# Kernel tuning notes

Hardware: AMD Instinct MI355X
Metric: run time of the kernel (lower is better)

The kernel has to match this reference:

```python
import jax, jax.numpy as jnp
import numpy as np

DECAY = 0.99
EPS = 1e-5  # Laplace smoothing eps in cluster-size balancing


def _quantize(z_flat, embedding, cluster_size, emb_avg, n_codes):
    # z_flat: [N, D]; embedding: [K, D]
    d = (jnp.sum(z_flat * z_flat, axis=1, keepdims=True)
         + jnp.sum(embedding * embedding, axis=1)
         - 2.0 * (z_flat @ embedding.T))                      # [N, K]
    idx = jnp.argmin(d, axis=1)                               # [N]
    # EMA update (training path). segment_sum == one-hot matmul scatter-add.
    counts = jax.ops.segment_sum(jnp.ones(z_flat.shape[0], z_flat.dtype), idx,
                                 num_segments=n_codes)        # [K]
    new_cs = cluster_size * DECAY + (1.0 - DECAY) * counts
    dw = jax.ops.segment_sum(z_flat, idx, num_segments=n_codes)  # [K, D]
    new_avg = emb_avg * DECAY + (1.0 - DECAY) * dw
    n = new_cs.sum()
    bal = (new_cs + EPS) / (n + n_codes * EPS) * n
    # torch assigns via .data (no autograd) -> stop_gradient for faithfulness
    new_emb = jax.lax.stop_gradient(new_avg / bal[:, None])
    z_q = jnp.take(new_emb, idx, axis=0)  # == one_hot(idx) @ new_emb
    return idx, z_q


def _l2norm(x):
    # F.normalize(x, dim=-1) with eps=1e-12
    return x / jnp.maximum(jnp.linalg.norm(x, axis=-1, keepdims=True), 1e-12)


def reference(z, structure_embedding, style_embedding,
              structure_cluster_size, style_cluster_size,
              structure_embedding_avg, style_embedding_avg):
    b, c, h, w, d = z.shape
    zp = jnp.transpose(z, (0, 2, 3, 4, 1))      # b h w d c
    z_flat = zp.reshape(-1, c)                  # [N, D]
    s_idx, s_q = _quantize(z_flat, structure_embedding, structure_cluster_size,
                           structure_embedding_avg, structure_embedding.shape[0])
    y_idx, y_q = _quantize(z_flat, style_embedding, style_cluster_size,
                           style_embedding_avg, style_embedding.shape[0])

    def back(q):  # [N, C] -> b c h w d
        return jnp.transpose(q.reshape(b, h, w, d, c), (0, 4, 1, 2, 3))

    s_enc = back(s_q)
    y_enc = back(y_q)
    # NOTE: faithful to source — normalize over LAST axis of (b,c,h,w,d),
    # i.e. the spatial depth axis, exactly as F.normalize(dim=-1) does there.
    dis = jnp.mean(jnp.sum(_l2norm(s_enc) * _l2norm(y_enc), axis=-1) ** 2)
    z_q = (s_enc + y_enc) * 0.5
    return z_q, dis, s_idx, y_idx


def setup_inputs() -> dict:
    key = jax.random.key(0)
    k1, k2, k3 = jax.random.split(key, 3)
    B, C, H, W, D = 16, 256, 16, 16, 16
    Ks, Ky = 1024, 512
    return {
        "z": jax.random.normal(k1, (B, C, H, W, D), dtype=jnp.float32),
        "structure_embedding": jax.random.normal(k2, (Ks, C), dtype=jnp.float32),
        "style_embedding": jax.random.normal(k3, (Ky, C), dtype=jnp.float32),
        "structure_cluster_size": jnp.zeros((Ks,), jnp.float32),
        "style_cluster_size": jnp.zeros((Ky,), jnp.float32),
        "structure_embedding_avg": jnp.zeros((Ks, C), jnp.float32),
        "style_embedding_avg": jnp.zeros((Ky, C), jnp.float32),
    }
```

## Files before the change

kernel.cpp:

```cpp
#include <hip/hip_runtime.h>
#include <float.h>

#define NROWS 65536
#define CDIM  256
#define KS    1024
#define KY    512
#define KTOT  1536
#define SPB   4096

#define WB_CNT_S       0
#define WB_CNT_Y       4096
#define WB_RESCUE_CNT  6144
#define WB_DISACC      6152
#define WB_DW_S        6400
#define WB_DW_Y        1054976
#define WB_ZERO_BYTES  1579264
#define WB_EIMG        1579264
#define WB_EN2         2365696
#define WB_IDXS_I      2371840
#define WB_IDXY_I      2633984
#define WB_RLIST_S     2896128
#define WB_RLIST_Y     3158272
#define WB_BASE_S      3420416
#define WB_BASE_Y      3424512
#define WB_CUR_S       3426560
#define WB_CUR_Y       3430656
#define WB_SCALE_S     3432704
#define WB_SCALE_Y     3436800
#define WB_PERM_S      3438848
#define WB_PERM_Y      3700992
#define WB_KSORT_S     3963136
#define WB_KSORT_Y     4225280
#define WB_EMB_S       4487424
#define WB_EMB_Y       5536000

#define OFF_OUT_ZQ   0
#define OFF_OUT_DIS  16777216
#define OFF_OUT_SIDX 16777217
#define OFF_OUT_YIDX 16842753

typedef __attribute__((ext_vector_type(8)))  _Float16 f16x8;
typedef __attribute__((ext_vector_type(4)))  float    f32x4;

__device__ __forceinline__ unsigned int umn(unsigned int a, unsigned int b) { return a < b ? a : b; }
__device__ __forceinline__ unsigned int umx(unsigned int a, unsigned int b) { return a > b ? a : b; }

__global__ void prep_e(const float* __restrict__ Es, const float* __restrict__ Ey,
                       unsigned short* __restrict__ eimg, float* __restrict__ en2) {
    int k = blockIdx.x;
    int lane = threadIdx.x;
    const float* E = (k < KS) ? (Es + (size_t)k * CDIM) : (Ey + (size_t)(k - KS) * CDIM);
    float4 v = *(const float4*)(E + lane * 4);
    float nrm = v.x * v.x + v.y * v.y + v.z * v.z + v.w * v.w;
#pragma unroll
    for (int off = 32; off > 0; off >>= 1) nrm += __shfl_down(nrm, off);
    if (lane == 0) en2[k] = nrm;

    unsigned short q0 = __builtin_bit_cast(unsigned short, (_Float16)v.x);
    unsigned short q1 = __builtin_bit_cast(unsigned short, (_Float16)v.y);
    unsigned short q2 = __builtin_bit_cast(unsigned short, (_Float16)v.z);
    unsigned short q3 = __builtin_bit_cast(unsigned short, (_Float16)v.w);
    uint2 hp = make_uint2((unsigned)q0 | ((unsigned)q1 << 16),
                          (unsigned)q2 | ((unsigned)q3 << 16));

    int c0 = lane * 4;
    int kc = c0 >> 5, g = (c0 >> 3) & 3, j0 = c0 & 7;
    size_t byteoff = (size_t)(k >> 4) * 8192 + (size_t)kc * 1024
                   + (size_t)(g * 16 + (k & 15)) * 16 + (size_t)j0 * 2;
    *(uint2*)((char*)eimg + byteoff) = hp;
}

__global__ void prep_z(const float* __restrict__ z, float* __restrict__ zf) {
    __shared__ float Zs[32][257];
    int blk = blockIdx.x;
    int n0 = blk * 32, b = n0 >> 12, s0 = n0 & 4095;
    int t = threadIdx.x;
    const float* zb = z + (size_t)b * CDIM * SPB + s0;
#pragma unroll
    for (int i = 0; i < 32; ++i) {
        int l = i * 256 + t;
        int c = l >> 5, s = l & 31;
        Zs[s][c] = zb[(size_t)c * SPB + s];
    }
    __syncthreads();
#pragma unroll
    for (int j = 0; j < 8; ++j) {
        int gid = j * 256 + t;
        int nl = gid >> 6, fg = gid & 63;
        float4 v = *(const float4*)(&Zs[nl][fg * 4]);
        *(float4*)(&zf[(size_t)(n0 + nl) * 256 + fg * 4]) = v;
    }
}

__device__ __forceinline__ void stage_phase(const unsigned short* __restrict__ eimg,
                                            int phase, char* lsbase, int wave, int lane) {
    const char* gs = (const char*)eimg + (size_t)phase * 16384 + (size_t)(wave * 2) * 1024 + lane * 16;
    char* ls = lsbase + wave * 2 * 1024;
#pragma unroll
    for (int i = 0; i < 2; ++i)
        __builtin_amdgcn_global_load_lds(
            (const __attribute__((address_space(1))) void*)(gs + i * 1024),
            (__attribute__((address_space(3))) void*)(ls + i * 1024), 16, 0, 0);
}

__launch_bounds__(512, 2)
__global__ void assign_kernel(const float* __restrict__ zf, const unsigned short* __restrict__ eimg,
                              const float* __restrict__ en2,
                              float* __restrict__ sidx_f, float* __restrict__ yidx_f,
                              int* __restrict__ sidx_i, int* __restrict__ yidx_i,
                              int* __restrict__ cnt_s, int* __restrict__ cnt_y,
                              int* __restrict__ rescue_cnt,
                              int* __restrict__ rlist_s, int* __restrict__ rlist_y) {
    __shared__ char sh[4][16384];
    const int tid = threadIdx.x, wave = tid >> 6, lane = tid & 63;
    const int n0 = blockIdx.x * 256;

    f16x8 A[2][8];
#pragma unroll
    for (int rg = 0; rg < 2; ++rg) {
        const float* zr = zf + (size_t)(n0 + wave * 32 + rg * 16 + (lane & 15)) * 256
                        + (lane >> 4) * 8;
#pragma unroll
        for (int kc = 0; kc < 8; ++kc) {
            float4 f0 = *(const float4*)(zr + kc * 32);
            float4 f1 = *(const float4*)(zr + kc * 32 + 4);
            f16x8 a;
            a[0] = (_Float16)f0.x; a[1] = (_Float16)f0.y;
            a[2] = (_Float16)f0.z; a[3] = (_Float16)f0.w;
            a[4] = (_Float16)f1.x; a[5] = (_Float16)f1.y;
            a[6] = (_Float16)f1.z; a[7] = (_Float16)f1.w;
            A[rg][kc] = a;
        }
    }

    stage_phase(eimg, 0, &sh[0][0], wave, lane);
    stage_phase(eimg, 1, &sh[1][0], wave, lane);

    unsigned int m1a[2][4], m2a[2][4];
#pragma unroll
    for (int rg = 0; rg < 2; ++rg)
#pragma unroll
        for (int q = 0; q < 4; ++q) { m1a[rg][q] = 0xFFFFFFFFu; m2a[rg][q] = 0xFFFFFFFFu; }

    for (int p = 0; p < 48; ++p) {
        if (p + 2 < 48) stage_phase(eimg, p + 2, &sh[(p + 2) & 3][0], wave, lane);
        if (p < 46)       asm volatile("s_waitcnt vmcnt(4)" ::: "memory");
        else if (p == 46) asm volatile("s_waitcnt vmcnt(2)" ::: "memory");
        else              asm volatile("s_waitcnt vmcnt(0)" ::: "memory");
        __builtin_amdgcn_s_barrier();
        asm volatile("" ::: "memory");

#pragma unroll
        for (int c = 0; c < 2; ++c) {
            const char* cb = &sh[p & 3][c * 8192] + lane * 16;
            f32x4 acc0 = {}, acc1 = {};
#pragma unroll
            for (int kc = 0; kc < 8; ++kc) {
                f16x8 B = *(const f16x8*)(cb + kc * 1024);
                acc0 = __builtin_amdgcn_mfma_f32_16x16x32_f16(A[0][kc], B, acc0, 0, 0, 0);
                acc1 = __builtin_amdgcn_mfma_f32_16x16x32_f16(A[1][kc], B, acc1, 0, 0, 0);
            }
            const int kcode = p * 32 + c * 16 + (lane & 15);
            const float en0 = en2[kcode] + 512.0f;
            const unsigned int tag = (unsigned int)kcode;
#pragma unroll
            for (int q = 0; q < 4; ++q) {
                float d0 = fmaf(-2.f, acc0[q], en0);
                unsigned int du0 = (__float_as_uint(d0) & 0xFFFFF800u) | tag;
                m2a[0][q] = umn(m2a[0][q], umx(m1a[0][q], du0));
                m1a[0][q] = umn(m1a[0][q], du0);
                float d1 = fmaf(-2.f, acc1[q], en0);
                unsigned int du1 = (__float_as_uint(d1) & 0xFFFFF800u) | tag;
                m2a[1][q] = umn(m2a[1][q], umx(m1a[1][q], du1));
                m1a[1][q] = umn(m1a[1][q], du1);
            }
        }

        if (p == 31) {
#pragma unroll
            for (int rg = 0; rg < 2; ++rg)
#pragma unroll
                for (int q = 0; q < 4; ++q) {
                    unsigned int v1 = m1a[rg][q], v2 = m2a[rg][q];
#pragma unroll
                    for (int m = 8; m >= 1; m >>= 1) {
                        unsigned int o1 = (unsigned int)__shfl_xor((int)v1, m);
                        unsigned int o2 = (unsigned int)__shfl_xor((int)v2, m);
                        v2 = umn(umn(v2, o2), umx(v1, o1));
                        v1 = umn(v1, o1);
                    }
                    if ((lane & 15) == 0) {
                        int kw = (int)(v1 & 0x7FFu);
                        int n = n0 + wave * 32 + rg * 16 + (lane >> 4) * 4 + q;
                        sidx_f[n] = (float)kw;
                        sidx_i[n] = kw;
                        atomicAdd(&cnt_s[kw], 1);
                        if ((v1 >> 11) + 4 > (v2 >> 11)) {
                            int k2w = (int)(v2 & 0x7FFu);
                            int pp = atomicAdd(&rescue_cnt[0], 1);
                            if (pp < 65536) rlist_s[pp] = n | (k2w << 16);
                        }
                    }
                    m1a[rg][q] = 0xFFFFFFFFu; m2a[rg][q] = 0xFFFFFFFFu;
                }
        }
    }

#pragma unroll
    for (int rg = 0; rg < 2; ++rg)
#pragma unroll
        for (int q = 0; q < 4; ++q) {
            unsigned int v1 = m1a[rg][q], v2 = m2a[rg][q];
#pragma unroll
            for (int m = 8; m >= 1; m >>= 1) {
                unsigned int o1 = (unsigned int)__shfl_xor((int)v1, m);
                unsigned int o2 = (unsigned int)__shfl_xor((int)v2, m);
                v2 = umn(umn(v2, o2), umx(v1, o1));
                v1 = umn(v1, o1);
            }
            if ((lane & 15) == 0) {
                int kw = (int)(v1 & 0x7FFu) - KS;
                int n = n0 + wave * 32 + rg * 16 + (lane >> 4) * 4 + q;
                yidx_f[n] = (float)kw;
                yidx_i[n] = kw;
                atomicAdd(&cnt_y[kw], 1);
                if ((v1 >> 11) + 4 > (v2 >> 11)) {
                    int k2w = (int)(v2 & 0x7FFu) - KS;
                    int pp = atomicAdd(&rescue_cnt[1], 1);
                    if (pp < 65536) rlist_y[pp] = n | (k2w << 16);
                }
            }
        }
}

__global__ void rescue2_kernel(const float* __restrict__ zf,
                               const float* __restrict__ Es, const float* __restrict__ Ey,
                               const float* __restrict__ en2, const int* __restrict__ rcnt,
                               const int* __restrict__ rlist_s, const int* __restrict__ rlist_y,
                               float* __restrict__ sidx_f, float* __restrict__ yidx_f,
                               int* __restrict__ sidx_i, int* __restrict__ yidx_i,
                               int* __restrict__ cnt_s, int* __restrict__ cnt_y) {
    int cs = rcnt[0]; if (cs > 65536) cs = 65536;
    int cy = rcnt[1]; if (cy > 65536) cy = 65536;
    int total = cs + cy;
    const int lane = threadIdx.x & 63;
    const int nw = (gridDim.x * blockDim.x) >> 6;
    for (int e = (int)((blockIdx.x * blockDim.x + threadIdx.x) >> 6); e < total; e += nw) {
        int book = (e >= cs);
        unsigned int ent = (unsigned int)(book ? rlist_y[e - cs] : rlist_s[e]);
        int n  = (int)(ent & 0xFFFFu);
        int k2 = (int)(ent >> 16);
        int* idx_i = book ? yidx_i : sidx_i;
        float* idx_f = book ? yidx_f : sidx_f;
        int* cnt = book ? cnt_y : cnt_s;
        const float* E = book ? Ey : Es;
        const float* en2k = book ? (en2 + KS) : en2;
        int k1 = idx_i[n];
        float4 zv = *(const float4*)(zf + (size_t)n * 256 + lane * 4);
        float4 a  = *(const float4*)(E + (size_t)k1 * 256 + lane * 4);
        float4 c  = *(const float4*)(E + (size_t)k2 * 256 + lane * 4);
        float d1 = zv.x * a.x + zv.y * a.y + zv.z * a.z + zv.w * a.w;
        float d2 = zv.x * c.x + zv.y * c.y + zv.z * c.z + zv.w * c.w;
#pragma unroll
        for (int off = 32; off > 0; off >>= 1) {
            d1 += __shfl_down(d1, off);
            d2 += __shfl_down(d2, off);
        }
        if (lane == 0) {
            float dist1 = en2k[k1] - 2.f * d1;
            float dist2 = en2k[k2] - 2.f * d2;
            int nk = (dist2 < dist1 || (dist2 == dist1 && k2 < k1)) ? k2 : k1;
            if (nk != k1) {
                atomicSub(&cnt[k1], 1);
                atomicAdd(&cnt[nk], 1);
                idx_i[n] = nk;
                idx_f[n] = (float)nk;
            }
        }
    }
}

__global__ void scanbal_kernel(const float* __restrict__ cs_in, const float* __restrict__ cy_in,
                               const int* __restrict__ cnt_s, const int* __restrict__ cnt_y,
                               int* __restrict__ base_s, int* __restrict__ base_y,
                               int* __restrict__ cur_s, int* __restrict__ cur_y,
                               float* __restrict__ scale_s, float* __restrict__ scale_y) {
    __shared__ int   sc[1024];
    __shared__ float sf[1024];
    int K = blockIdx.x ? KY : KS;
    const float* csi = blockIdx.x ? cy_in : cs_in;
    const int*   cnt = blockIdx.x ? cnt_y : cnt_s;
    int* base = blockIdx.x ? base_y : base_s;
    int* cur  = blockIdx.x ? cur_y  : cur_s;
    float* scale = blockIdx.x ? scale_y : scale_s;
    int t = threadIdx.x;
    int c = (t < K) ? cnt[t] : 0;
    float ncs = (t < K) ? (csi[t] * 0.99f + 0.01f * (float)c) : 0.f;
    sc[t] = c;
    __syncthreads();
    for (int off = 1; off < 1024; off <<= 1) {
        int v = sc[t] + ((t >= off) ? sc[t - off] : 0);
        __syncthreads();
        sc[t] = v;
        __syncthreads();
    }
    int incl = sc[t];
    sf[t] = ncs;
    __syncthreads();
    for (int s2 = 512; s2 > 0; s2 >>= 1) {
        if (t < s2) sf[t] += sf[t + s2];
        __syncthreads();
    }
    float nsum = sf[0];
    if (t < K) {
        base[t] = incl - c;
        cur[t]  = incl - c;
        float bal = (ncs + 1e-5f) / (nsum + (float)K * 1e-5f) * nsum;
        scale[t] = 1.0f / bal;
    }
}

__global__ void scatter_kernel(const int* __restrict__ si, const int* __restrict__ yi,
                               int* __restrict__ cur_s, int* __restrict__ cur_y,
                               int* __restrict__ perm_s, int* __restrict__ perm_y,
                               int* __restrict__ ksort_s, int* __restrict__ ksort_y) {
    int i = blockIdx.x * 256 + threadIdx.x;
    if (i < NROWS) {
        int k = si[i]; int p = atomicAdd(&cur_s[k], 1);
        perm_s[p] = i; ksort_s[p] = k;
    } else {
        int n = i - NROWS; int k = yi[n]; int p = atomicAdd(&cur_y[k], 1);
        perm_y[p] = n; ksort_y[p] = k;
    }
}

__global__ void dw_kernel(const float* __restrict__ zf,
                          const int* __restrict__ perm_s, const int* __restrict__ ksort_s,
                          const int* __restrict__ perm_y, const int* __restrict__ ksort_y,
                          float* __restrict__ dw_s, float* __restrict__ dw_y) {
    __shared__ int keys[33];
    __shared__ int rows[32];
    const int t = threadIdx.x;
    int blk = blockIdx.x;
    const int* perm; const int* ks; float* dw; int p0;
    if (blk < NROWS / 32) { perm = perm_s; ks = ksort_s; dw = dw_s; p0 = blk * 32; }
    else                  { perm = perm_y; ks = ksort_y; dw = dw_y; p0 = (blk - NROWS / 32) * 32; }
    if (t < 32) { keys[t] = ks[p0 + t]; rows[t] = perm[p0 + t]; }
    if (t == 32) keys[32] = -1;
    __syncthreads();
    float acc = 0.f;
#pragma unroll 8
    for (int j = 0; j < 32; ++j) {
        acc += zf[(size_t)rows[j] * 256 + t];
        if (keys[j + 1] != keys[j]) {
            atomicAdd(&dw[(size_t)keys[j] * 256 + t], acc);
            acc = 0.f;
        }
    }
}

__global__ void embnew_kernel(const float* __restrict__ avg_s, const float* __restrict__ avg_y,
                              const float* __restrict__ dw_s, const float* __restrict__ dw_y,
                              const float* __restrict__ scale_s, const float* __restrict__ scale_y,
                              float* __restrict__ emb_s, float* __restrict__ emb_y) {
    int id = blockIdx.x, t = threadIdx.x;
    if (id < KS) { int i = id * 256 + t; emb_s[i] = (avg_s[i] * 0.99f + 0.01f * dw_s[i]) * scale_s[id]; }
    else { int kk = id - KS; int i = kk * 256 + t; emb_y[i] = (avg_y[i] * 0.99f + 0.01f * dw_y[i]) * scale_y[kk]; }
}

__global__ void gather_kernel(const float* __restrict__ Se, const float* __restrict__ Ye,
                              const int* __restrict__ sidx, const int* __restrict__ yidx,
                              float* __restrict__ zq, float* __restrict__ disacc) {
    __shared__ float qb[256 * 17];
    __shared__ int   si[16], yi[16];
    __shared__ float red[256];
    const int g  = blockIdx.x;
    const int b  = g >> 8;
    const int hw = g & 255;
    const int t  = threadIdx.x;
    if (t < 16) {
        int n = b * SPB + hw * 16 + t;
        si[t] = sidx[n];
        yi[t] = yidx[n];
    }
    __syncthreads();
    float ns = 0.f, ny = 0.f, dot = 0.f;
#pragma unroll
    for (int d = 0; d < 16; ++d) {
        float s = Se[(size_t)si[d] * CDIM + t];
        float y = Ye[(size_t)yi[d] * CDIM + t];
        ns  = fmaf(s, s, ns);
        ny  = fmaf(y, y, ny);
        dot = fmaf(s, y, dot);
        qb[t * 17 + d] = 0.5f * (s + y);
    }
    float den = fmaxf(sqrtf(ns), 1e-12f) * fmaxf(sqrtf(ny), 1e-12f);
    float val = dot / den;
    red[t] = val * val;
    __syncthreads();
    for (int s = 128; s > 0; s >>= 1) {
        if (t < s) red[t] += red[t + s];
        __syncthreads();
    }
    if (t == 0) atomicAdd(disacc, red[0]);
    float* zg = zq + (size_t)b * CDIM * SPB + hw * 16;
#pragma unroll
    for (int j = 0; j < 16; ++j) {
        int e = j * 256 + t;
        int c = e >> 4, d = e & 15;
        zg[(size_t)c * SPB + d] = qb[c * 17 + d];
    }
}

__global__ void fin_kernel(const float* __restrict__ disacc, float* __restrict__ out_dis) {
    *out_dis = *disacc * (1.0f / 1048576.0f);
}

extern "C" void kernel_launch(void* const* d_in, const int* in_sizes, int n_in,
                              void* d_out, int out_size, void* d_ws, size_t ws_size,
                              hipStream_t stream) {
    const float* z     = (const float*)d_in[0];
    const float* Es    = (const float*)d_in[1];
    const float* Ey    = (const float*)d_in[2];
    const float* s_cs  = (const float*)d_in[3];
    const float* y_cs  = (const float*)d_in[4];
    const float* s_avg = (const float*)d_in[5];
    const float* y_avg = (const float*)d_in[6];
    float* out = (float*)d_out;
    char*  w   = (char*)d_ws;

    unsigned short* eimg = (unsigned short*)(w + WB_EIMG);
    float* en2    = (float*)(w + WB_EN2);
    int* idxs_i   = (int*)(w + WB_IDXS_I);
    int* idxy_i   = (int*)(w + WB_IDXY_I);
    int* cnt_s    = (int*)(w + WB_CNT_S);
    int* cnt_y    = (int*)(w + WB_CNT_Y);
    int* r_cnt    = (int*)(w + WB_RESCUE_CNT);
    int* rlist_s  = (int*)(w + WB_RLIST_S);
    int* rlist_y  = (int*)(w + WB_RLIST_Y);
    int* base_s   = (int*)(w + WB_BASE_S);
    int* base_y   = (int*)(w + WB_BASE_Y);
    int* cur_s    = (int*)(w + WB_CUR_S);
    int* cur_y    = (int*)(w + WB_CUR_Y);
    float* scale_s = (float*)(w + WB_SCALE_S);
    float* scale_y = (float*)(w + WB_SCALE_Y);
    int* perm_s   = (int*)(w + WB_PERM_S);
    int* perm_y   = (int*)(w + WB_PERM_Y);
    int* ksort_s  = (int*)(w + WB_KSORT_S);
    int* ksort_y  = (int*)(w + WB_KSORT_Y);
    float* dw_s   = (float*)(w + WB_DW_S);
    float* dw_y   = (float*)(w + WB_DW_Y);
    float* emb_s  = (float*)(w + WB_EMB_S);
    float* emb_y  = (float*)(w + WB_EMB_Y);

    float* zf     = out + OFF_OUT_ZQ;
    float* sidx_f = out + OFF_OUT_SIDX;
    float* yidx_f = out + OFF_OUT_YIDX;

    hipMemsetAsync(w, 0, WB_ZERO_BYTES, stream);

    prep_e<<<KTOT, 64, 0, stream>>>(Es, Ey, eimg, en2);
    prep_z<<<NROWS / 32, 256, 0, stream>>>(z, zf);

    assign_kernel<<<NROWS / 256, 512, 0, stream>>>(zf, eimg, en2, sidx_f, yidx_f,
                                                   idxs_i, idxy_i, cnt_s, cnt_y,
                                                   r_cnt, rlist_s, rlist_y);

    rescue2_kernel<<<512, 256, 0, stream>>>(zf, Es, Ey, en2, r_cnt, rlist_s, rlist_y,
                                            sidx_f, yidx_f, idxs_i, idxy_i, cnt_s, cnt_y);

    scanbal_kernel<<<2, 1024, 0, stream>>>(s_cs, y_cs, cnt_s, cnt_y, base_s, base_y,
                                           cur_s, cur_y, scale_s, scale_y);
    scatter_kernel<<<2 * NROWS / 256, 256, 0, stream>>>(idxs_i, idxy_i, cur_s, cur_y,
                                                        perm_s, perm_y, ksort_s, ksort_y);
    dw_kernel<<<2 * NROWS / 32, 256, 0, stream>>>(zf, perm_s, ksort_s, perm_y, ksort_y, dw_s, dw_y);
    embnew_kernel<<<KTOT, 256, 0, stream>>>(s_avg, y_avg, dw_s, dw_y, scale_s, scale_y, emb_s, emb_y);
    gather_kernel<<<4096, 256, 0, stream>>>(emb_s, emb_y, idxs_i, idxy_i,
                                            out + OFF_OUT_ZQ, (float*)(w + WB_DISACC));
    fin_kernel<<<1, 1, 0, stream>>>((float*)(w + WB_DISACC), out + OFF_OUT_DIS);
}
```

Before: 327.7 us.

## Load codebook fragments directly into registers instead of LDS staging in assign kernel

The assign kernel previously staged codebook tiles into shared memory with async global-to-LDS loads, a 4-deep ring and block-wide barriers. Now each wave loads its B fragments straight from global memory (L2-cached) into registers, double-buffered in software, with no LDS and no barriers. Blocks shrink to 256 threads, 128 rows each. This removes barrier stalls and LDS traffic but makes every wave fetch the whole codebook from cache, raising L2 bandwidth demand and register pressure.

```diff
diff --git a/kernel.cpp b/kernel.cpp
--- a/kernel.cpp
+++ b/kernel.cpp
@@ -92,18 +92,69 @@
     }
 }
 
-__device__ __forceinline__ void stage_phase(const unsigned short* __restrict__ eimg,
-                                            int phase, char* lsbase, int wave, int lane) {
-    const char* gs = (const char*)eimg + (size_t)phase * 16384 + (size_t)(wave * 2) * 1024 + lane * 16;
-    char* ls = lsbase + wave * 2 * 1024;
-#pragma unroll
-    for (int i = 0; i < 2; ++i)
-        __builtin_amdgcn_global_load_lds(
-            (const __attribute__((address_space(1))) void*)(gs + i * 1024),
-            (__attribute__((address_space(3))) void*)(ls + i * 1024), 16, 0, 0);
-}
-
-__launch_bounds__(512, 2)
+#define LOADB(Bd, t_)                                                          \
+    {                                                                          \
+        const char* gb = (const char*)eimg + (size_t)(t_) * 8192 + lane16;     \
+        _Pragma("unroll")                                                      \
+        for (int kc = 0; kc < 8; ++kc)                                         \
+            Bd[kc] = *(const f16x8*)(gb + kc * 1024);                          \
+    }
+
+#define COMPUTE(Bd, t_)                                                        \
+    {                                                                          \
+        f32x4 acc0 = {}, acc1 = {};                                            \
+        _Pragma("unroll")                                                      \
+        for (int kc = 0; kc < 8; ++kc) {                                       \
+            acc0 = __builtin_amdgcn_mfma_f32_16x16x32_f16(A[0][kc], Bd[kc], acc0, 0, 0, 0); \
+            acc1 = __builtin_amdgcn_mfma_f32_16x16x32_f16(A[1][kc], Bd[kc], acc1, 0, 0, 0); \
+        }                                                                      \
+        const int kcode = (t_) * 16 + (lane & 15);                             \
+        const float en0 = en2[kcode] + 512.0f;                                 \
+        const unsigned int tag = (unsigned int)kcode;                          \
+        _Pragma("unroll")                                                      \
+        for (int q = 0; q < 4; ++q) {                                          \
+            float d0 = fmaf(-2.f, acc0[q], en0);                               \
+            unsigned int du0 = (__float_as_uint(d0) & 0xFFFFF800u) | tag;      \
+            m2a[0][q] = umn(m2a[0][q], umx(m1a[0][q], du0));                   \
+            m1a[0][q] = umn(m1a[0][q], du0);                                   \
+            float d1 = fmaf(-2.f, acc1[q], en0);                               \
+            unsigned int du1 = (__float_as_uint(d1) & 0xFFFFF800u) | tag;      \
+            m2a[1][q] = umn(m2a[1][q], umx(m1a[1][q], du1));                   \
+            m1a[1][q] = umn(m1a[1][q], du1);                                   \
+        }                                                                      \
+    }
+
+#define FLUSH(book, fo, io, cb, rl)                                            \
+    {                                                                          \
+        _Pragma("unroll")                                                      \
+        for (int rg = 0; rg < 2; ++rg)                                         \
+        _Pragma("unroll")                                                      \
+        for (int q = 0; q < 4; ++q) {                                          \
+            unsigned int v1 = m1a[rg][q], v2 = m2a[rg][q];                     \
+            _Pragma("unroll")                                                  \
+            for (int m = 8; m >= 1; m >>= 1) {                                 \
+                unsigned int o1 = (unsigned int)__shfl_xor((int)v1, m);        \
+                unsigned int o2 = (unsigned int)__shfl_xor((int)v2, m);        \
+                v2 = umn(umn(v2, o2), umx(v1, o1));                            \
+                v1 = umn(v1, o1);                                              \
+            }                                                                  \
+            if ((lane & 15) == 0) {                                            \
+                int kw = (int)(v1 & 0x7FFu) - ((book) ? KS : 0);               \
+                int n = n0 + rg * 16 + (lane >> 4) * 4 + q;                    \
+                fo[n] = (float)kw;                                             \
+                io[n] = kw;                                                    \
+                atomicAdd(&cb[kw], 1);                                         \
+                if ((v1 >> 11) + 4 > (v2 >> 11)) {                             \
+                    int k2w = (int)(v2 & 0x7FFu) - ((book) ? KS : 0);          \
+                    int pp = atomicAdd(&rescue_cnt[book], 1);                  \
+                    if (pp < 65536) rl[pp] = n | (k2w << 16);                  \
+                }                                                              \
+            }                                                                  \
+            m1a[rg][q] = 0xFFFFFFFFu; m2a[rg][q] = 0xFFFFFFFFu;                \
+        }                                                                      \
+    }
+
+__launch_bounds__(256, 2)
 __global__ void assign_kernel(const float* __restrict__ zf, const unsigned short* __restrict__ eimg,
                               const float* __restrict__ en2,
                               float* __restrict__ sidx_f, float* __restrict__ yidx_f,
@@ -111,15 +162,14 @@
                               int* __restrict__ cnt_s, int* __restrict__ cnt_y,
                               int* __restrict__ rescue_cnt,
                               int* __restrict__ rlist_s, int* __restrict__ rlist_y) {
-    __shared__ char sh[4][16384];
     const int tid = threadIdx.x, wave = tid >> 6, lane = tid & 63;
-    const int n0 = blockIdx.x * 256;
+    const int n0 = blockIdx.x * 128 + wave * 32;
+    const size_t lane16 = (size_t)(lane * 16);
 
     f16x8 A[2][8];
 #pragma unroll
     for (int rg = 0; rg < 2; ++rg) {
-        const float* zr = zf + (size_t)(n0 + wave * 32 + rg * 16 + (lane & 15)) * 256
-                        + (lane >> 4) * 8;
+        const float* zr = zf + (size_t)(n0 + rg * 16 + (lane & 15)) * 256 + (lane >> 4) * 8;
 #pragma unroll
         for (int kc = 0; kc < 8; ++kc) {
             float4 f0 = *(const float4*)(zr + kc * 32);
@@ -133,104 +183,32 @@
         }
     }
 
-    stage_phase(eimg, 0, &sh[0][0], wave, lane);
-    stage_phase(eimg, 1, &sh[1][0], wave, lane);
-
     unsigned int m1a[2][4], m2a[2][4];
 #pragma unroll
     for (int rg = 0; rg < 2; ++rg)
 #pragma unroll
         for (int q = 0; q < 4; ++q) { m1a[rg][q] = 0xFFFFFFFFu; m2a[rg][q] = 0xFFFFFFFFu; }
 
-    for (int p = 0; p < 48; ++p) {
-        if (p + 2 < 48) stage_phase(eimg, p + 2, &sh[(p + 2) & 3][0], wave, lane);
-        if (p < 46)       asm volatile("s_waitcnt vmcnt(4)" ::: "memory");
-        else if (p == 46) asm volatile("s_waitcnt vmcnt(2)" ::: "memory");
-        else              asm volatile("s_waitcnt vmcnt(0)" ::: "memory");
-        __builtin_amdgcn_s_barrier();
-        asm volatile("" ::: "memory");
-
-#pragma unroll
-        for (int c = 0; c < 2; ++c) {
-            const char* cb = &sh[p & 3][c * 8192] + lane * 16;
-            f32x4 acc0 = {}, acc1 = {};
-#pragma unroll
-            for (int kc = 0; kc < 8; ++kc) {
-                f16x8 B = *(const f16x8*)(cb + kc * 1024);
-                acc0 = __builtin_amdgcn_mfma_f32_16x16x32_f16(A[0][kc], B, acc0, 0, 0, 0);
-                acc1 = __builtin_amdgcn_mfma_f32_16x16x32_f16(A[1][kc], B, acc1, 0, 0, 0);
-            }
-            const int kcode = p * 32 + c * 16 + (lane & 15);
-            const float en0 = en2[kcode] + 512.0f;
-            const unsigned int tag = (unsigned int)kcode;
-#pragma unroll
-            for (int q = 0; q < 4; ++q) {
-                float d0 = fmaf(-2.f, acc0[q], en0);
-                unsigned int du0 = (__float_as_uint(d0) & 0xFFFFF800u) | tag;
-                m2a[0][q] = umn(m2a[0][q], umx(m1a[0][q], du0));
-                m1a[0][q] = umn(m1a[0][q], du0);
-                float d1 = fmaf(-2.f, acc1[q], en0);
-                unsigned int du1 = (__float_as_uint(d1) & 0xFFFFF800u) | tag;
-                m2a[1][q] = umn(m2a[1][q], umx(m1a[1][q], du1));
-                m1a[1][q] = umn(m1a[1][q], du1);
-            }
-        }
-
-        if (p == 31) {
-#pragma unroll
-            for (int rg = 0; rg < 2; ++rg)
-#pragma unroll
-                for (int q = 0; q < 4; ++q) {
-                    unsigned int v1 = m1a[rg][q], v2 = m2a[rg][q];
-#pragma unroll
-                    for (int m = 8; m >= 1; m >>= 1) {
-                        unsigned int o1 = (unsigned int)__shfl_xor((int)v1, m);
-                        unsigned int o2 = (unsigned int)__shfl_xor((int)v2, m);
-                        v2 = umn(umn(v2, o2), umx(v1, o1));
-                        v1 = umn(v1, o1);
-                    }
-                    if ((lane & 15) == 0) {
-                        int kw = (int)(v1 & 0x7FFu);
-                        int n = n0 + wave * 32 + rg * 16 + (lane >> 4) * 4 + q;
-                        sidx_f[n] = (float)kw;
-                        sidx_i[n] = kw;
-                        atomicAdd(&cnt_s[kw], 1);
-                        if ((v1 >> 11) + 4 > (v2 >> 11)) {
-                            int k2w = (int)(v2 & 0x7FFu);
-                            int pp = atomicAdd(&rescue_cnt[0], 1);
-                            if (pp < 65536) rlist_s[pp] = n | (k2w << 16);
-                        }
-                    }
-                    m1a[rg][q] = 0xFFFFFFFFu; m2a[rg][q] = 0xFFFFFFFFu;
-                }
-        }
-    }
-
-#pragma unroll
-    for (int rg = 0; rg < 2; ++rg)
-#pragma unroll
-        for (int q = 0; q < 4; ++q) {
-            unsigned int v1 = m1a[rg][q], v2 = m2a[rg][q];
-#pragma unroll
-            for (int m = 8; m >= 1; m >>= 1) {
-                unsigned int o1 = (unsigned int)__shfl_xor((int)v1, m);
-                unsigned int o2 = (unsigned int)__shfl_xor((int)v2, m);
-                v2 = umn(umn(v2, o2), umx(v1, o1));
-                v1 = umn(v1, o1);
-            }
-            if ((lane & 15) == 0) {
-                int kw = (int)(v1 & 0x7FFu) - KS;
-                int n = n0 + wave * 32 + rg * 16 + (lane >> 4) * 4 + q;
-                yidx_f[n] = (float)kw;
-                yidx_i[n] = kw;
-                atomicAdd(&cnt_y[kw], 1);
-                if ((v1 >> 11) + 4 > (v2 >> 11)) {
-                    int k2w = (int)(v2 & 0x7FFu) - KS;
-                    int pp = atomicAdd(&rescue_cnt[1], 1);
-                    if (pp < 65536) rlist_y[pp] = n | (k2w << 16);
-                }
-            }
-        }
+    f16x8 B0[8], B1[8];
+    LOADB(B0, 0);
+
+#pragma unroll 1
+    for (int t = 0; t < 64; t += 2) {
+        LOADB(B1, t + 1);
+        COMPUTE(B0, t);
+        LOADB(B0, t + 2);
+        COMPUTE(B1, t + 1);
+    }
+    FLUSH(0, sidx_f, sidx_i, cnt_s, rlist_s);
+
+#pragma unroll 1
+    for (int t = 64; t < 96; t += 2) {
+        LOADB(B1, t + 1);
+        COMPUTE(B0, t);
+        if (t + 2 < 96) LOADB(B0, t + 2);
+        COMPUTE(B1, t + 1);
+    }
+    FLUSH(1, yidx_f, yidx_i, cnt_y, rlist_y);
 }
 
 __global__ void rescue2_kernel(const float* __restrict__ zf,
@@ -462,7 +440,7 @@
     prep_e<<<KTOT, 64, 0, stream>>>(Es, Ey, eimg, en2);
     prep_z<<<NROWS / 32, 256, 0, stream>>>(z, zf);
 
-    assign_kernel<<<NROWS / 256, 512, 0, stream>>>(zf, eimg, en2, sidx_f, yidx_f,
+    assign_kernel<<<NROWS / 128, 256, 0, stream>>>(zf, eimg, en2, sidx_f, yidx_f,
                                                    idxs_i, idxy_i, cnt_s, cnt_y,
                                                    r_cnt, rlist_s, rlist_y);
 
```

After: 316.1 us. -3.6%, faster.
